# Optimization experiments

Hardware: AMD Instinct MI355X
Metric: run time of the kernel (lower is better)

## Reference

```python
import jax, jax.numpy as jnp
import numpy as np

N_NODES = 50000
N_EDGES = 800000
N_S = 32          # 0e channels in node feats
N_V = 16          # 1o channels in node feats
NB = 8            # radial bessel basis size
H = 64            # MLP hidden
S_OUT = N_S + N_V           # 48 scalar message channels (filtered 0e + dot path)
V_OUT = N_V + N_S + N_V     # 64 vector message channels (filtered 1o + sxY1 + vxY2)
NUM_IRREPS = S_OUT + V_OUT  # 112, gated by radial MLP
AVG_NEIGH = 16.0


def setup_inputs() -> dict:
    key = jax.random.key(0)
    ks = jax.random.split(key, 8)
    # scale so edge lengths fall mostly inside the envelope cutoff x_max=1
    vectors = jax.random.normal(ks[0], (N_EDGES, 3), jnp.float32) * 0.25
    node_s = jax.random.normal(ks[1], (N_NODES, N_S), jnp.float32)
    node_v = jax.random.normal(ks[2], (N_NODES, N_V, 3), jnp.float32)
    senders = jax.random.randint(ks[3], (N_EDGES,), 0, N_NODES)
    receivers = jax.random.randint(ks[4], (N_EDGES,), 0, N_NODES)
    W0 = jax.random.normal(ks[5], (NB, H), jnp.float32)
    W1 = jax.random.normal(ks[6], (H, H), jnp.float32)
    W2 = jax.random.normal(ks[7], (H, NUM_IRREPS), jnp.float32)
    return {"vectors": vectors, "node_s": node_s, "node_v": node_v,
            "W0": W0, "W1": W1, "W2": W2,
            "senders": senders, "receivers": receivers}


def _radial_embed(r):
    # r: [E,1] edge lengths. Bessel basis (x_max=1) * polynomial envelope, 0 at r==0.
    n = jnp.arange(1, NB + 1, dtype=r.dtype)            # [NB]
    safe_r = jnp.maximum(r, 1e-12)
    basis = jnp.sqrt(2.0) * jnp.sin(jnp.pi * n * r) / safe_r   # [E,NB]
    x = r
    env = (1.0 - 28.0 * x**6 + 48.0 * x**7 - 21.0 * x**8) * (x < 1.0)  # smooth cutoff
    return jnp.where(r == 0.0, 0.0, basis * env)        # [E,NB]


def reference(vectors, node_s, node_v, W0, W1, W2, senders, receivers):
    E = vectors.shape[0]
    r = jnp.linalg.norm(vectors, axis=-1, keepdims=True)          # [E,1]
    u = vectors / jnp.maximum(r, 1e-12)                            # unit vectors [E,3]

    # gather sender features
    s = node_s[senders]                                            # [E,N_S]
    v = node_v[senders]                                            # [E,N_V,3]

    # equivariant tensor-product paths against spherical harmonics of u
    # (filtered to target irreps 0e,1o). Y1 ~ u, Y2 ~ traceless u u^T.
    path_a = s[:, :, None] * u[:, None, :]                         # 0e x Y1 -> 1o [E,N_S,3]
    path_b = jnp.einsum('eci,ei->ec', v, u)                        # 1o x Y1 -> 0e [E,N_V]
    T = u[:, :, None] * u[:, None, :] - jnp.eye(3, dtype=u.dtype) / 3.0  # [E,3,3]
    path_c = jnp.sqrt(1.5) * jnp.einsum('eij,ecj->eci', T, v)      # 1o x Y2 -> 1o [E,N_V,3]

    msg_s = jnp.concatenate([s, path_b], axis=-1)                  # [E,S_OUT]
    msg_v = jnp.concatenate([v, path_a, path_c], axis=1)           # [E,V_OUT,3]

    # radial MLP gate (no bias, fan-in scaled, swish hidden, linear output)
    emb = _radial_embed(r)                                         # [E,NB]
    h = jax.nn.swish(emb @ W0 / jnp.sqrt(jnp.asarray(NB, emb.dtype)))
    h = jax.nn.swish(h @ W1 / jnp.sqrt(jnp.asarray(H, emb.dtype)))
    mix = h @ W2 / jnp.sqrt(jnp.asarray(H, emb.dtype))             # [E,NUM_IRREPS]

    msg_s = msg_s * mix[:, :S_OUT]
    msg_v = msg_v * mix[:, S_OUT:, None]

    # scatter-add to receivers
    n = node_s.shape[0]
    out_s = jnp.zeros((n, S_OUT), msg_s.dtype).at[receivers].add(msg_s)
    out_v = jnp.zeros((n, V_OUT, 3), msg_v.dtype).at[receivers].add(msg_v)

    inv = 1.0 / jnp.sqrt(AVG_NEIGH)
    return jnp.concatenate([out_s * inv, (out_v * inv).reshape(n, V_OUT * 3)], axis=-1)
```

## Files before the change

### kernel.cpp

```cpp
#include <hip/hip_runtime.h>
#include <hip/hip_fp16.h>

#define N_S 32
#define N_V 16
#define NB 8
#define HH 64
#define NIR 112
#define ROW 240
#define MROW 120

typedef _Float16 half8 __attribute__((ext_vector_type(8)));
typedef float f32x4 __attribute__((ext_vector_type(4)));

__device__ __forceinline__ float swishf(float x) {
  return x / (1.f + __expf(-x));
}

struct ChanDesc { int path, off, mixI, i; };

__device__ __forceinline__ void mkDesc(int t, ChanDesc& d) {
  if (t < 32) { d.path = 0; d.off = t; d.mixI = t; d.i = 0; }
  else if (t < 48) { d.path = 1; d.off = 3 * (t - 32); d.mixI = t; d.i = 0; }
  else if (t < ROW) {
    int q = t - 48, c = q / 3, i = q - 3 * c;
    d.mixI = 48 + c;
    if (c < 16) { d.path = 2; d.off = q; d.i = 0; }
    else if (c < 48) { d.path = 3; d.off = c - 16; d.i = i; }
    else { d.path = 4; d.off = 3 * (c - 48); d.i = i; }
  } else { d.path = -1; d.off = 0; d.mixI = 0; d.i = 0; }
}

__device__ __forceinline__ float evalChan(const ChanDesc& d,
                                          const float* __restrict__ srow,
                                          const float* __restrict__ vrow,
                                          float mix, float u0, float u1, float u2) {
  if (d.path < 0) return 0.f;
  if (d.path == 0) return srow[d.off] * mix;
  if (d.path == 2) return vrow[d.off] * mix;
  float uo = d.i == 0 ? u0 : (d.i == 1 ? u1 : u2);
  if (d.path == 3) return srow[d.off] * uo * mix;
  float dd = vrow[d.off] * u0 + vrow[d.off + 1] * u1 + vrow[d.off + 2] * u2;
  if (d.path == 1) return dd * mix;
  return 1.22474487139f * (uo * dd - vrow[d.off + d.i] * 0.33333333333f) * mix;
}

__device__ __forceinline__ float evalChan16(const ChanDesc& d,
                                            const _Float16* __restrict__ srow,
                                            const _Float16* __restrict__ vrow,
                                            float mix, float u0, float u1, float u2) {
  if (d.path == 0) return (float)srow[d.off] * mix;
  if (d.path == 2) return (float)vrow[d.off] * mix;
  float uo = d.i == 0 ? u0 : (d.i == 1 ? u1 : u2);
  if (d.path == 3) return (float)srow[d.off] * uo * mix;
  float dd = (float)vrow[d.off] * u0 + (float)vrow[d.off + 1] * u1 + (float)vrow[d.off + 2] * u2;
  if (d.path == 1) return dd * mix;
  return 1.22474487139f * (uo * dd - (float)vrow[d.off + d.i] * 0.33333333333f) * mix;
}

__device__ __forceinline__ void radialEmb(float x, float y, float z, bool valid,
                                          float* emb, float* u0, float* u1, float* u2) {
  float r2 = x * x + y * y + z * z;
  float r = sqrtf(r2);
  float invr = 1.f / fmaxf(r, 1e-12f);
  *u0 = x * invr; *u1 = y * invr; *u2 = z * invr;
  float env = 0.f;
  if (r < 1.f) {
    float r3 = r * r2;
    float r6 = r3 * r3;
    env = 1.f + r6 * (-28.f + (48.f - 21.f * r) * r);
  }
  float coef = 1.41421356237f * invr * env;
  if (!valid || r == 0.f) coef = 0.f;
  float ph = 3.14159265358979323846f * r;
  float s1 = __sinf(ph), c1 = __cosf(ph);
  float twc = 2.f * c1;
  float sp = 0.f, sc = s1;
#pragma unroll
  for (int n = 0; n < NB; ++n) {
    emb[n] = coef * sc;
    float sn = twc * sc - sp;
    sp = sc;
    sc = sn;
  }
}


__global__ __launch_bounds__(256) void hist_kernel(const int* __restrict__ rcv,
                                                   int* __restrict__ hist, int E) {
  int e = blockIdx.x * 256 + threadIdx.x;
  if (e < E) atomicAdd(&hist[rcv[e]], 1);
}

__global__ __launch_bounds__(256) void scan1_kernel(const int* __restrict__ hist,
                                                    int* __restrict__ scanTmp,
                                                    int* __restrict__ bsum, int N) {
  __shared__ int sh[256];
  int t = threadIdx.x;
  int i = blockIdx.x * 256 + t;
  sh[t] = (i < N) ? hist[i] : 0;
  __syncthreads();
#pragma unroll
  for (int off = 1; off < 256; off <<= 1) {
    int x = (t >= off) ? sh[t - off] : 0;
    __syncthreads();
    sh[t] += x;
    __syncthreads();
  }
  if (i < N) scanTmp[i] = sh[t];
  if (t == 255) bsum[blockIdx.x] = sh[255];
}

__global__ __launch_bounds__(256) void scan2_kernel(int* __restrict__ bsum, int nb) {
  __shared__ int sh[256];
  int t = threadIdx.x;
  sh[t] = (t < nb) ? bsum[t] : 0;
  __syncthreads();
#pragma unroll
  for (int off = 1; off < 256; off <<= 1) {
    int x = (t >= off) ? sh[t - off] : 0;
    __syncthreads();
    sh[t] += x;
    __syncthreads();
  }
  int excl = (t == 0) ? 0 : sh[t - 1];
  if (t < nb) bsum[t] = excl;
}

__global__ __launch_bounds__(256) void scan3_kernel(const int* __restrict__ scanTmp,
                                                    const int* __restrict__ bsum,
                                                    const int* __restrict__ hist,
                                                    int* __restrict__ offs,
                                                    int* __restrict__ cursor, int N) {
  int i = blockIdx.x * 256 + threadIdx.x;
  if (i < N) {
    int incl = scanTmp[i] + bsum[blockIdx.x];
    offs[i + 1] = incl;
    cursor[i] = incl - hist[i];
    if (i == 0) offs[0] = 0;
  }
}

__global__ __launch_bounds__(256) void reorder_kernel(const int* __restrict__ rcv,
                                                      int* __restrict__ cursor,
                                                      int* __restrict__ sortedE, int E) {
  int e = blockIdx.x * 256 + threadIdx.x;
  if (e < E) {
    int pos = atomicAdd(&cursor[rcv[e]], 1);
    sortedE[pos] = e;
  }
}

__global__ __launch_bounds__(256) void reorderInv_kernel(const int* __restrict__ rcv,
                                                         int* __restrict__ cursor,
                                                         int* __restrict__ invPos, int E) {
  int e = blockIdx.x * 256 + threadIdx.x;
  if (e < E) {
    int pos = atomicAdd(&cursor[rcv[e]], 1);
    invPos[e] = pos;
  }
}


__global__ __launch_bounds__(256) void wconv2_kernel(const float* __restrict__ W1,
                                                     const float* __restrict__ W2,
                                                     _Float16* __restrict__ W1T,
                                                     _Float16* __restrict__ W2T) {
  int i = blockIdx.x * 256 + threadIdx.x;
  if (i < 4096) {
    int k = i >> 6, n = i & 63;
    W1T[n * 64 + k] = (_Float16)(W1[k * 64 + n] * 0.125f);
  } else if (i < 4096 + 7168) {
    int j = i - 4096;
    int k = j / 112, n = j - k * 112;
    W2T[n * 64 + k] = (_Float16)(W2[k * 112 + n] * 0.125f);
  }
}

__global__ __launch_bounds__(256) void nodeconv_kernel(const float* __restrict__ ns,
                                                       const float* __restrict__ nv,
                                                       _Float16* __restrict__ s16,
                                                       _Float16* __restrict__ v16, int N) {
  int i = blockIdx.x * 256 + threadIdx.x;
  int ts = N * N_S;
  int tv = N * N_V * 3;
  if (i < ts) s16[i] = (_Float16)ns[i];
  else if (i < ts + tv) v16[i - ts] = (_Float16)nv[i - ts];
}

__global__ __launch_bounds__(256, 4) void mlp_mfma_sorted_kernel(
    const float* __restrict__ vec,
    const float* __restrict__ W0,
    const _Float16* __restrict__ W1T,
    const _Float16* __restrict__ W2T,
    const int* __restrict__ senders,
    const int* __restrict__ invPos,
    _Float16* __restrict__ mixS,
    int E) {
  __shared__ __align__(16) _Float16 hbuf[4 * 64 * 72];
  const int lane = threadIdx.x & 63;
  const int wave = threadIdx.x >> 6;
  const int gbase = blockIdx.x * 256 + wave * 64;
  _Float16* hb = hbuf + wave * (64 * 72);

  const int m15 = lane & 15;
  const int q = lane >> 4;

  {
    int e = gbase + lane;
    bool valid = e < E;
    float x = 0.f, y = 0.f, z = 0.f;
    int snd = 0;
    if (valid) {
      const float* vp = vec + 3 * (size_t)e;
      x = vp[0]; y = vp[1]; z = vp[2];
      snd = senders[e];
    }
    float emb[NB], u0, u1, u2;
    radialEmb(x, y, z, valid, emb, &u0, &u1, &u2);
    for (int kg = 0; kg < 8; ++kg) {
      half8 pk;
#pragma unroll
      for (int kk = 0; kk < 8; ++kk) {
        int k = kg * 8 + kk;
        float a = 0.f;
#pragma unroll
        for (int n = 0; n < NB; ++n) a = fmaf(emb[n], W0[n * HH + k], a);
        pk[kk] = (_Float16)swishf(a * 0.35355339059f);
      }
      *(half8*)(hb + lane * 72 + kg * 8) = pk;
    }
    float* auxp = (float*)(hb + lane * 72 + 64);
    auxp[0] = u0; auxp[1] = u1; auxp[2] = u2;
    ((int*)auxp)[3] = snd;
  }

  half8 bW1[4][2];
#pragma unroll
  for (int nt = 0; nt < 4; ++nt)
#pragma unroll
    for (int q2 = 0; q2 < 2; ++q2)
      bW1[nt][q2] = *(const half8*)(W1T + (nt * 16 + m15) * 64 + q2 * 32 + q * 8);

#pragma unroll
  for (int t = 0; t < 4; ++t) {
    half8 a0 = *(const half8*)(hb + (t * 16 + m15) * 72 + q * 8);
    half8 a1 = *(const half8*)(hb + (t * 16 + m15) * 72 + 32 + q * 8);
#pragma unroll
    for (int nt = 0; nt < 4; ++nt) {
      f32x4 d = {0.f, 0.f, 0.f, 0.f};
      d = __builtin_amdgcn_mfma_f32_16x16x32_f16(a0, bW1[nt][0], d, 0, 0, 0);
      d = __builtin_amdgcn_mfma_f32_16x16x32_f16(a1, bW1[nt][1], d, 0, 0, 0);
#pragma unroll
      for (int r = 0; r < 4; ++r)
        hb[(t * 16 + q * 4 + r) * 72 + nt * 16 + m15] = (_Float16)swishf(d[r]);
    }
  }

  half8 A2[4][2];
#pragma unroll
  for (int t = 0; t < 4; ++t)
#pragma unroll
    for (int q2 = 0; q2 < 2; ++q2)
      A2[t][q2] = *(const half8*)(hb + (t * 16 + m15) * 72 + q2 * 32 + q * 8);

  for (int nl = 0; nl < 4; ++nl) {
    half8 b0 = *(const half8*)(W2T + (nl * 16 + m15) * 64 + q * 8);
    half8 b1 = *(const half8*)(W2T + (nl * 16 + m15) * 64 + 32 + q * 8);
#pragma unroll
    for (int t = 0; t < 4; ++t) {
      f32x4 d = {0.f, 0.f, 0.f, 0.f};
      d = __builtin_amdgcn_mfma_f32_16x16x32_f16(A2[t][0], b0, d, 0, 0, 0);
      d = __builtin_amdgcn_mfma_f32_16x16x32_f16(A2[t][1], b1, d, 0, 0, 0);
#pragma unroll
      for (int r = 0; r < 4; ++r)
        hb[(t * 16 + q * 4 + r) * 72 + nl * 16 + m15] = (_Float16)d[r];
    }
  }
  for (int it = 0; it < 8; ++it) {
    int c = it * 64 + lane;
    int el = c >> 3, p = c & 7;
    int e = gbase + el;
    half8 v = *(const half8*)(hb + el * 72 + p * 8);
    if (e < E) {
      int pos = invPos[e];
      *(half8*)(mixS + (size_t)pos * MROW + p * 8) = v;
    }
  }

  for (int nl = 0; nl < 3; ++nl) {
    int ntg = 4 + nl;
    half8 b0 = *(const half8*)(W2T + (ntg * 16 + m15) * 64 + q * 8);
    half8 b1 = *(const half8*)(W2T + (ntg * 16 + m15) * 64 + 32 + q * 8);
#pragma unroll
    for (int t = 0; t < 4; ++t) {
      f32x4 d = {0.f, 0.f, 0.f, 0.f};
      d = __builtin_amdgcn_mfma_f32_16x16x32_f16(A2[t][0], b0, d, 0, 0, 0);
      d = __builtin_amdgcn_mfma_f32_16x16x32_f16(A2[t][1], b1, d, 0, 0, 0);
#pragma unroll
      for (int r = 0; r < 4; ++r)
        hb[(t * 16 + q * 4 + r) * 72 + nl * 16 + m15] = (_Float16)d[r];
    }
  }
  for (int it = 0; it < 7; ++it) {
    int c = it * 64 + lane;
    int el = (int)(((unsigned)c * 9363u) >> 16);
    int p = c - el * 7;
    int e = gbase + el;
    half8 v = *(const half8*)(hb + el * 72 + (p < 6 ? p * 8 : 64));
    if (e < E) {
      int pos = invPos[e];
      *(half8*)(mixS + (size_t)pos * MROW + 64 + p * 8) = v;
    }
  }
}


__device__ __forceinline__ void gstep(int i, const _Float16* __restrict__ mixS,
                                      const _Float16* __restrict__ s16,
                                      const _Float16* __restrict__ v16,
                                      const ChanDesc* __restrict__ d, float* __restrict__ acc) {
  const _Float16* row = mixS + (size_t)i * MROW;
  float4 aux = *(const float4*)(const void*)(row + 112);
  int snd = __float_as_int(aux.w);
  const _Float16* srow = s16 + (size_t)snd * N_S;
  const _Float16* vrow = v16 + (size_t)snd * (N_V * 3);
#pragma unroll
  for (int tb = 0; tb < 4; ++tb) {
    if (d[tb].path >= 0) {
      float m = (float)row[d[tb].mixI];
      acc[tb] += evalChan16(d[tb], srow, vrow, m, aux.x, aux.y, aux.z);
    }
  }
}

__global__ __launch_bounds__(256) void gather_sorted_kernel(
    const _Float16* __restrict__ mixS,
    const _Float16* __restrict__ s16,
    const _Float16* __restrict__ v16,
    const int* __restrict__ offs,
    float* __restrict__ out, int N) {
  int wid = blockIdx.x * 4 + (threadIdx.x >> 6);
  int lane = threadIdx.x & 63;
  if (wid >= N) return;

  ChanDesc d[4];
#pragma unroll
  for (int tb = 0; tb < 4; ++tb) mkDesc(tb * 64 + lane, d[tb]);

  float acc[4] = {0.f, 0.f, 0.f, 0.f};
  int s0 = __builtin_amdgcn_readfirstlane(offs[wid]);
  int s1 = __builtin_amdgcn_readfirstlane(offs[wid + 1]);

  int i = s0;
  for (; i + 2 <= s1; i += 2) {
    gstep(i, mixS, s16, v16, d, acc);
    gstep(i + 1, mixS, s16, v16, d, acc);
  }
  if (i < s1) gstep(i, mixS, s16, v16, d, acc);

  float* orow = out + (size_t)wid * ROW;
#pragma unroll
  for (int tb = 0; tb < 4; ++tb) {
    int t = tb * 64 + lane;
    if (t < ROW) orow[t] = 0.25f * acc[tb];
  }
}


__global__ __launch_bounds__(256, 4) void mlp_mfma_kernel(
    const float* __restrict__ vec,
    const float* __restrict__ W0,
    const _Float16* __restrict__ W1T,
    const _Float16* __restrict__ W2T,
    __half* __restrict__ mixOut, int E) {
  __shared__ __align__(16) _Float16 hbuf[4 * 64 * 72];
  const int lane = threadIdx.x & 63;
  const int wave = threadIdx.x >> 6;
  const int gbase = blockIdx.x * 256 + wave * 64;
  _Float16* hb = hbuf + wave * (64 * 72);
  const int m15 = lane & 15;
  const int q = lane >> 4;

  {
    int e = gbase + lane;
    bool valid = e < E;
    float x = 0.f, y = 0.f, z = 0.f;
    if (valid) {
      const float* vp = vec + 3 * (size_t)e;
      x = vp[0]; y = vp[1]; z = vp[2];
    }
    float emb[NB], u0, u1, u2;
    radialEmb(x, y, z, valid, emb, &u0, &u1, &u2);
    for (int kg = 0; kg < 8; ++kg) {
      half8 pk;
#pragma unroll
      for (int kk = 0; kk < 8; ++kk) {
        int k = kg * 8 + kk;
        float a = 0.f;
#pragma unroll
        for (int n = 0; n < NB; ++n) a = fmaf(emb[n], W0[n * HH + k], a);
        pk[kk] = (_Float16)swishf(a * 0.35355339059f);
      }
      *(half8*)(hb + lane * 72 + kg * 8) = pk;
    }
  }

  half8 bW1[4][2];
#pragma unroll
  for (int nt = 0; nt < 4; ++nt)
#pragma unroll
    for (int q2 = 0; q2 < 2; ++q2)
      bW1[nt][q2] = *(const half8*)(W1T + (nt * 16 + m15) * 64 + q2 * 32 + q * 8);

#pragma unroll
  for (int t = 0; t < 4; ++t) {
    half8 a0 = *(const half8*)(hb + (t * 16 + m15) * 72 + q * 8);
    half8 a1 = *(const half8*)(hb + (t * 16 + m15) * 72 + 32 + q * 8);
#pragma unroll
    for (int nt = 0; nt < 4; ++nt) {
      f32x4 d = {0.f, 0.f, 0.f, 0.f};
      d = __builtin_amdgcn_mfma_f32_16x16x32_f16(a0, bW1[nt][0], d, 0, 0, 0);
      d = __builtin_amdgcn_mfma_f32_16x16x32_f16(a1, bW1[nt][1], d, 0, 0, 0);
#pragma unroll
      for (int r = 0; r < 4; ++r)
        hb[(t * 16 + q * 4 + r) * 72 + nt * 16 + m15] = (_Float16)swishf(d[r]);
    }
  }

  half8 A2[4][2];
#pragma unroll
  for (int t = 0; t < 4; ++t)
#pragma unroll
    for (int q2 = 0; q2 < 2; ++q2)
      A2[t][q2] = *(const half8*)(hb + (t * 16 + m15) * 72 + q2 * 32 + q * 8);

  for (int hf = 0; hf < 2; ++hf) {
    const int ntCount = hf ? 3 : 4;
    for (int nl = 0; nl < ntCount; ++nl) {
      int ntg = hf * 4 + nl;
      half8 b0 = *(const half8*)(W2T + (ntg * 16 + m15) * 64 + q * 8);
      half8 b1 = *(const half8*)(W2T + (ntg * 16 + m15) * 64 + 32 + q * 8);
#pragma unroll
      for (int t = 0; t < 4; ++t) {
        f32x4 d = {0.f, 0.f, 0.f, 0.f};
        d = __builtin_amdgcn_mfma_f32_16x16x32_f16(A2[t][0], b0, d, 0, 0, 0);
        d = __builtin_amdgcn_mfma_f32_16x16x32_f16(A2[t][1], b1, d, 0, 0, 0);
#pragma unroll
        for (int r = 0; r < 4; ++r)
          hb[(t * 16 + q * 4 + r) * 72 + nl * 16 + m15] = (_Float16)d[r];
      }
    }
    if (hf == 0) {
      for (int it = 0; it < 8; ++it) {
        int c = it * 64 + lane;
        int el = c >> 3, p = c & 7;
        int e = gbase + el;
        half8 v = *(const half8*)(hb + el * 72 + p * 8);
        if (e < E) *(half8*)((_Float16*)mixOut + (size_t)e * NIR + p * 8) = v;
      }
    } else {
      for (int it = 0; it < 6; ++it) {
        int c = it * 64 + lane;
        int el = (int)(((unsigned)c * 43691u) >> 18);
        int p = c - el * 6;
        int e = gbase + el;
        half8 v = *(const half8*)(hb + el * 72 + p * 8);
        if (e < E) *(half8*)((_Float16*)mixOut + (size_t)e * NIR + 64 + p * 8) = v;
      }
    }
  }
}

__global__ __launch_bounds__(256) void gather_kernel(
    const float* __restrict__ vec,
    const float* __restrict__ nodes_s,
    const float* __restrict__ nodes_v,
    const int* __restrict__ senders,
    const int* __restrict__ offs,
    const int* __restrict__ sortedE,
    const __half* __restrict__ mix,
    float* __restrict__ out, int N) {
  int wid = blockIdx.x * 4 + (threadIdx.x >> 6);
  int lane = threadIdx.x & 63;
  if (wid >= N) return;

  ChanDesc d[4];
#pragma unroll
  for (int tb = 0; tb < 4; ++tb) mkDesc(tb * 64 + lane, d[tb]);

  float acc[4] = {0.f, 0.f, 0.f, 0.f};
  int s0 = offs[wid], s1 = offs[wid + 1];

  for (int i = s0; i < s1; ++i) {
    int e = __builtin_amdgcn_readfirstlane(sortedE[i]);
    int snd = __builtin_amdgcn_readfirstlane(senders[e]);
    const float* vp = vec + 3 * (size_t)e;
    float x = vp[0], y = vp[1], z = vp[2];
    float r = sqrtf(x * x + y * y + z * z);
    float invr = 1.f / fmaxf(r, 1e-12f);
    float u0 = x * invr, u1 = y * invr, u2 = z * invr;
    const float* srow = nodes_s + (size_t)snd * N_S;
    const float* vrow = nodes_v + (size_t)snd * (N_V * 3);
    const __half* mrow = mix + (size_t)e * NIR;
#pragma unroll
    for (int tb = 0; tb < 4; ++tb) {
      if (d[tb].path >= 0) {
        float m = __half2float(mrow[d[tb].mixI]);
        acc[tb] += evalChan(d[tb], srow, vrow, m, u0, u1, u2);
      }
    }
  }

  float* orow = out + (size_t)wid * ROW;
#pragma unroll
  for (int tb = 0; tb < 4; ++tb) {
    int t = tb * 64 + lane;
    if (t < ROW) orow[t] = 0.25f * acc[tb];
  }
}


__global__ __launch_bounds__(64) void edge_kernel(
    const float* __restrict__ vec,
    const float* __restrict__ nodes_s,
    const float* __restrict__ nodes_v,
    const int* __restrict__ senders,
    const int* __restrict__ receivers,
    const float* __restrict__ W0f,
    const float* __restrict__ W1f,
    const float* __restrict__ W2f,
    float* __restrict__ out, int E) {
  __shared__ float hLds[HH * 64];
  __shared__ float uLds[64 * 3];
  __shared__ int sLds[64];
  __shared__ int rLds[64];
  __half* mixLds = reinterpret_cast<__half*>(hLds);

  const int lane = threadIdx.x;
  const int base = blockIdx.x * 64;
  const int eg = base + lane;
  const bool valid = eg < E;

  float emb[NB];
  {
    float x = 0.f, y = 0.f, z = 0.f;
    int snd = 0, rcv = 0;
    if (valid) {
      const float* vp = vec + 3 * (size_t)eg;
      x = vp[0]; y = vp[1]; z = vp[2];
      snd = senders[eg];
      rcv = receivers[eg];
    }
    float u0, u1, u2;
    radialEmb(x, y, z, valid, emb, &u0, &u1, &u2);
    uLds[lane * 3 + 0] = u0;
    uLds[lane * 3 + 1] = u1;
    uLds[lane * 3 + 2] = u2;
    sLds[lane] = snd;
    rLds[lane] = rcv;
  }

  for (int j0 = 0; j0 < HH; j0 += 8) {
    float a[8];
#pragma unroll
    for (int jj = 0; jj < 8; ++jj) a[jj] = 0.f;
#pragma unroll
    for (int k = 0; k < NB; ++k) {
      const float* wrow = W0f + k * HH + j0;
      float ek = emb[k];
#pragma unroll
      for (int jj = 0; jj < 8; ++jj) a[jj] = fmaf(ek, wrow[jj], a[jj]);
    }
#pragma unroll
    for (int jj = 0; jj < 8; ++jj)
      hLds[(j0 + jj) * 64 + lane] = swishf(a[jj] * 0.35355339059f);
  }
  __syncthreads();

  float h2[HH];
#pragma unroll
  for (int j = 0; j < HH; ++j) h2[j] = 0.f;
  for (int k = 0; k < HH; ++k) {
    float hk = hLds[k * 64 + lane];
    const float* wrow = W1f + k * HH;
#pragma unroll
    for (int j = 0; j < HH; ++j) h2[j] = fmaf(hk, wrow[j], h2[j]);
  }
#pragma unroll
  for (int j = 0; j < HH; ++j) h2[j] = swishf(h2[j] * 0.125f);
  __syncthreads();

  for (int m0 = 0; m0 < NIR; m0 += 4) {
    float a0 = 0.f, a1 = 0.f, a2 = 0.f, a3 = 0.f;
#pragma unroll
    for (int k = 0; k < HH; ++k) {
      const float* wrow = W2f + k * NIR + m0;
      float hk = h2[k];
      a0 = fmaf(hk, wrow[0], a0);
      a1 = fmaf(hk, wrow[1], a1);
      a2 = fmaf(hk, wrow[2], a2);
      a3 = fmaf(hk, wrow[3], a3);
    }
    mixLds[lane * NIR + m0 + 0] = __float2half_rn(a0 * 0.125f);
    mixLds[lane * NIR + m0 + 1] = __float2half_rn(a1 * 0.125f);
    mixLds[lane * NIR + m0 + 2] = __float2half_rn(a2 * 0.125f);
    mixLds[lane * NIR + m0 + 3] = __float2half_rn(a3 * 0.125f);
  }
  __syncthreads();

  ChanDesc d[4];
#pragma unroll
  for (int tb = 0; tb < 4; ++tb) mkDesc(tb * 64 + lane, d[tb]);

  const int cnt = min(64, E - base);
  for (int e = 0; e < cnt; ++e) {
    int snd = sLds[e], rcv = rLds[e];
    float u0 = uLds[e * 3 + 0], u1 = uLds[e * 3 + 1], u2 = uLds[e * 3 + 2];
    const float* srow = nodes_s + (size_t)snd * N_S;
    const float* vrow = nodes_v + (size_t)snd * (N_V * 3);
    const __half* mrow = mixLds + e * NIR;
    float* orow = out + (size_t)rcv * ROW;
#pragma unroll
    for (int tb = 0; tb < 4; ++tb) {
      if (d[tb].path >= 0) {
        float m = __half2float(mrow[d[tb].mixI]);
        float val = evalChan(d[tb], srow, vrow, m, u0, u1, u2);
        unsafeAtomicAdd(orow + tb * 64 + lane, 0.25f * val);
      }
    }
  }
}


extern "C" void kernel_launch(void* const* d_in, const int* in_sizes, int n_in,
                              void* d_out, int out_size, void* d_ws, size_t ws_size,
                              hipStream_t stream) {
  const float* vec = (const float*)d_in[0];
  const float* ns = (const float*)d_in[1];
  const float* nv = (const float*)d_in[2];
  const float* w0 = (const float*)d_in[3];
  const float* w1 = (const float*)d_in[4];
  const float* w2 = (const float*)d_in[5];
  const int* snd = (const int*)d_in[6];
  const int* rcv = (const int*)d_in[7];
  float* out = (float*)d_out;

  const int E = in_sizes[6];
  const int N = in_sizes[1] / N_S;
  const int nb = (N + 255) / 256;
  const int eb = (E + 255) / 256;

  {
    char* p = (char*)d_ws;
    _Float16* mixS = (_Float16*)p; p += (size_t)E * MROW * sizeof(_Float16);
    int* hist = (int*)p;           p += (size_t)N * 4;
    int* scanTmp = (int*)p;        p += (size_t)N * 4;
    int* offs = (int*)p;           p += ((size_t)N + 1) * 4;
    int* cursor = (int*)p;         p += (size_t)N * 4;
    int* bsum = (int*)p;           p += 256 * 4;
    int* invPos = (int*)p;         p += (size_t)E * 4;
    p = (char*)(((uintptr_t)p + 15) & ~(uintptr_t)15);
    _Float16* W1T = (_Float16*)p;  p += 4096 * sizeof(_Float16);
    _Float16* W2T = (_Float16*)p;  p += 7168 * sizeof(_Float16);
    _Float16* s16 = (_Float16*)p;  p += (size_t)N * N_S * sizeof(_Float16);
    _Float16* v16 = (_Float16*)p;  p += (size_t)N * N_V * 3 * sizeof(_Float16);
    size_t needA = (size_t)(p - (char*)d_ws);

    if (needA <= ws_size && nb <= 256) {
      hipMemsetAsync(hist, 0, (size_t)N * 4, stream);
      hist_kernel<<<eb, 256, 0, stream>>>(rcv, hist, E);
      scan1_kernel<<<nb, 256, 0, stream>>>(hist, scanTmp, bsum, N);
      scan2_kernel<<<1, 256, 0, stream>>>(bsum, nb);
      scan3_kernel<<<nb, 256, 0, stream>>>(scanTmp, bsum, hist, offs, cursor, N);
      reorderInv_kernel<<<eb, 256, 0, stream>>>(rcv, cursor, invPos, E);
      wconv2_kernel<<<44, 256, 0, stream>>>(w1, w2, W1T, W2T);
      nodeconv_kernel<<<(N * 80 + 255) / 256, 256, 0, stream>>>(ns, nv, s16, v16, N);
      mlp_mfma_sorted_kernel<<<eb, 256, 0, stream>>>(vec, w0, W1T, W2T, snd, invPos, mixS, E);
      gather_sorted_kernel<<<(N + 3) / 4, 256, 0, stream>>>(mixS, s16, v16, offs, out, N);
      return;
    }
  }

  {
    char* p = (char*)d_ws;
    __half* mixW = (__half*)p;     p += (size_t)E * NIR * sizeof(__half);
    int* hist = (int*)p;           p += (size_t)N * 4;
    int* scanTmp = (int*)p;        p += (size_t)N * 4;
    int* offs = (int*)p;           p += ((size_t)N + 1) * 4;
    int* cursor = (int*)p;         p += (size_t)N * 4;
    int* bsum = (int*)p;           p += 256 * 4;
    int* sortedE = (int*)p;        p += (size_t)E * 4;
    p = (char*)(((uintptr_t)p + 15) & ~(uintptr_t)15);
    _Float16* W1T = (_Float16*)p;  p += 4096 * sizeof(_Float16);
    _Float16* W2T = (_Float16*)p;  p += 7168 * sizeof(_Float16);
    size_t needB = (size_t)(p - (char*)d_ws);

    if (needB <= ws_size && nb <= 256) {
      hipMemsetAsync(hist, 0, (size_t)N * 4, stream);
      hist_kernel<<<eb, 256, 0, stream>>>(rcv, hist, E);
      scan1_kernel<<<nb, 256, 0, stream>>>(hist, scanTmp, bsum, N);
      scan2_kernel<<<1, 256, 0, stream>>>(bsum, nb);
      scan3_kernel<<<nb, 256, 0, stream>>>(scanTmp, bsum, hist, offs, cursor, N);
      reorder_kernel<<<eb, 256, 0, stream>>>(rcv, cursor, sortedE, E);
      wconv2_kernel<<<44, 256, 0, stream>>>(w1, w2, W1T, W2T);
      mlp_mfma_kernel<<<eb, 256, 0, stream>>>(vec, w0, W1T, W2T, mixW, E);
      gather_kernel<<<(N + 3) / 4, 256, 0, stream>>>(vec, ns, nv, snd, offs, sortedE, mixW, out, N);
      return;
    }
  }

  hipMemsetAsync(d_out, 0, (size_t)out_size * sizeof(float), stream);
  edge_kernel<<<(E + 63) / 64, 64, 0, stream>>>(vec, ns, nv, snd, rcv, w0, w1, w2, out, E);
}
```

Measured before the change: 661.4 us.

## Stage sorted edge mix rows and sender features in LDS for gather kernel

Replaces the per-wave gather kernel, where each lane read mix rows and sender node features directly from global memory per edge, with a block-level kernel. The block cooperatively loads up to 64 edges' mix rows and sender feature rows into shared memory using 16-byte vector loads, then each wave accumulates its receiver's edges from LDS. The aim is coalesced, wide global loads instead of scattered per-lane half loads. It adds three barriers per chunk, and waves whose receivers have few edges wait on the others.

Result: faster. 561.7 us (-15.1%).

```diff
diff --git a/kernel.cpp b/kernel.cpp
--- a/kernel.cpp
+++ b/kernel.cpp
@@ -8,6 +8,7 @@
 #define NIR 112
 #define ROW 240
 #define MROW 120
+#define GCAP 64
 
 typedef _Float16 half8 __attribute__((ext_vector_type(8)));
 typedef float f32x4 __attribute__((ext_vector_type(4)));
@@ -186,6 +187,7 @@
   if (i < ts) s16[i] = (_Float16)ns[i];
   else if (i < ts + tv) v16[i - ts] = (_Float16)nv[i - ts];
 }
+
 
 __global__ __launch_bounds__(256, 4) void mlp_mfma_sorted_kernel(
     const float* __restrict__ vec,
@@ -314,55 +316,76 @@
   }
 }
 
-
-__device__ __forceinline__ void gstep(int i, const _Float16* __restrict__ mixS,
-                                      const _Float16* __restrict__ s16,
-                                      const _Float16* __restrict__ v16,
-                                      const ChanDesc* __restrict__ d, float* __restrict__ acc) {
-  const _Float16* row = mixS + (size_t)i * MROW;
-  float4 aux = *(const float4*)(const void*)(row + 112);
-  int snd = __float_as_int(aux.w);
-  const _Float16* srow = s16 + (size_t)snd * N_S;
-  const _Float16* vrow = v16 + (size_t)snd * (N_V * 3);
-#pragma unroll
-  for (int tb = 0; tb < 4; ++tb) {
-    if (d[tb].path >= 0) {
-      float m = (float)row[d[tb].mixI];
-      acc[tb] += evalChan16(d[tb], srow, vrow, m, aux.x, aux.y, aux.z);
-    }
-  }
-}
-
-__global__ __launch_bounds__(256) void gather_sorted_kernel(
+__global__ __launch_bounds__(256) void gather_lds_kernel(
     const _Float16* __restrict__ mixS,
     const _Float16* __restrict__ s16,
     const _Float16* __restrict__ v16,
     const int* __restrict__ offs,
     float* __restrict__ out, int N) {
-  int wid = blockIdx.x * 4 + (threadIdx.x >> 6);
-  int lane = threadIdx.x & 63;
-  if (wid >= N) return;
+  __shared__ __align__(16) _Float16 mixLds[GCAP * MROW];
+  __shared__ __align__(16) _Float16 nodeLds[GCAP * 80];
+
+  const int tid = threadIdx.x;
+  const int lane = tid & 63;
+  const int wave = tid >> 6;
+  const int wid0 = blockIdx.x * 4;
+
+  const int e0 = offs[wid0];
+  const int e4 = offs[min(wid0 + 4, N)];
+  const int wid = wid0 + wave;
+  const int sw = offs[min(wid, N)];
+  const int ew = offs[min(wid + 1, N)];
 
   ChanDesc d[4];
 #pragma unroll
   for (int tb = 0; tb < 4; ++tb) mkDesc(tb * 64 + lane, d[tb]);
 
   float acc[4] = {0.f, 0.f, 0.f, 0.f};
-  int s0 = __builtin_amdgcn_readfirstlane(offs[wid]);
-  int s1 = __builtin_amdgcn_readfirstlane(offs[wid + 1]);
-
-  int i = s0;
-  for (; i + 2 <= s1; i += 2) {
-    gstep(i, mixS, s16, v16, d, acc);
-    gstep(i + 1, mixS, s16, v16, d, acc);
-  }
-  if (i < s1) gstep(i, mixS, s16, v16, d, acc);
-
-  float* orow = out + (size_t)wid * ROW;
-#pragma unroll
-  for (int tb = 0; tb < 4; ++tb) {
-    int t = tb * 64 + lane;
-    if (t < ROW) orow[t] = 0.25f * acc[tb];
+
+  for (int c0 = e0; c0 < e4; c0 += GCAP) {
+    const int cnt = min(GCAP, e4 - c0);
+    for (int ch = tid; ch < cnt * 15; ch += 256) {
+      int row = ch / 15, part = ch - row * 15;
+      *(half8*)(mixLds + row * MROW + part * 8) =
+          *(const half8*)(mixS + (size_t)(c0 + row) * MROW + part * 8);
+    }
+    __syncthreads();
+    for (int ch = tid; ch < cnt * 10; ch += 256) {
+      int row = ch / 10, part = ch - row * 10;
+      int snd = ((const int*)(mixLds + row * MROW + 112))[3];
+      const _Float16* src = (part < 4)
+          ? s16 + (size_t)snd * N_S + part * 8
+          : v16 + (size_t)snd * (N_V * 3) + (part - 4) * 8;
+      *(half8*)(nodeLds + row * 80 + (part < 4 ? part * 8 : 32 + (part - 4) * 8)) =
+          *(const half8*)src;
+    }
+    __syncthreads();
+    const int jlo = max(sw - c0, 0);
+    const int jhi = min(ew - c0, cnt);
+    for (int j = jlo; j < jhi; ++j) {
+      const _Float16* row = mixLds + j * MROW;
+      const float* aux = (const float*)(row + 112);
+      float u0 = aux[0], u1 = aux[1], u2 = aux[2];
+      const _Float16* srow = nodeLds + j * 80;
+      const _Float16* vrow = srow + 32;
+#pragma unroll
+      for (int tb = 0; tb < 4; ++tb) {
+        if (d[tb].path >= 0) {
+          float m = (float)row[d[tb].mixI];
+          acc[tb] += evalChan16(d[tb], srow, vrow, m, u0, u1, u2);
+        }
+      }
+    }
+    __syncthreads();
+  }
+
+  if (wid < N) {
+    float* orow = out + (size_t)wid * ROW;
+#pragma unroll
+    for (int tb = 0; tb < 4; ++tb) {
+      int t = tb * 64 + lane;
+      if (t < ROW) orow[t] = 0.25f * acc[tb];
+    }
   }
 }
 
@@ -676,7 +699,7 @@
       wconv2_kernel<<<44, 256, 0, stream>>>(w1, w2, W1T, W2T);
       nodeconv_kernel<<<(N * 80 + 255) / 256, 256, 0, stream>>>(ns, nv, s16, v16, N);
       mlp_mfma_sorted_kernel<<<eb, 256, 0, stream>>>(vec, w0, W1T, W2T, snd, invPos, mixS, E);
-      gather_sorted_kernel<<<(N + 3) / 4, 256, 0, stream>>>(mixS, s16, v16, offs, out, N);
+      gather_lds_kernel<<<(N + 3) / 4, 256, 0, stream>>>(mixS, s16, v16, offs, out, N);
       return;
     }
   }
```
